# Kernel tuning notes

Measured on AMD Instinct MI355X. Metric: run time of the kernel, lower is better.

Reference implementation:

```python
import jax, jax.numpy as jnp
import numpy as np
import math

SR = 48000       # sample_rate
SEG = 960        # segment_size
NH = 8           # num_harmonics
BASE_F = 220.0   # base_frequency


def _interp_linear(v, Lw):
    # torch F.interpolate(mode='linear', align_corners=False) from (N,C,Lf) -> (N,C,Lw)
    Lf = v.shape[-1]
    pos = (jnp.arange(Lw, dtype=jnp.float32) + 0.5) * (Lf / Lw) - 0.5
    pos = jnp.clip(pos, 0.0, Lf - 1)
    i0 = jnp.floor(pos).astype(jnp.int32)
    i1 = jnp.minimum(i0 + 1, Lf - 1)
    w = (pos - i0.astype(jnp.float32))
    return v[..., i0] * (1.0 - w) + v[..., i1] * w


def setup_inputs() -> dict:
    key = jax.random.key(0)
    k = jax.random.split(key, 4)
    N, C, Lf = 32, 256, 250
    x = jax.random.normal(k[0], (N, C, Lf), jnp.float32)
    phi = jax.random.normal(k[1], (N, 1, 1), jnp.float32)
    # 1x1 Conv1d weights (out, in, 1); small scale keeps f0/mag in a sane range
    w_mag = jax.random.normal(k[2], (NH, C, 1), jnp.float32) * 0.02
    b_mag = jnp.zeros((NH,), jnp.float32)
    w_oct = jax.random.normal(k[3], (1, C, 1), jnp.float32) * 0.02
    b_oct = jnp.zeros((1,), jnp.float32)
    return dict(x=x, phi=phi, w_mag=w_mag, b_mag=b_mag, w_oct=w_oct, b_oct=b_oct)


def reference(x, phi, w_mag, b_mag, w_oct, b_oct):
    N, C, Lf = x.shape
    Lw = Lf * SEG
    # 1x1 conv = channel matmul
    octave = jnp.einsum('oc,ncl->nol', w_oct[:, :, 0], x) + b_oct[None, :, None]   # (N,1,Lf)
    mag = jnp.exp(jnp.minimum(
        jnp.einsum('oc,ncl->nol', w_mag[:, :, 0], x) + b_mag[None, :, None], 6.0))  # (N,NH,Lf)
    f0 = BASE_F * jnp.exp2(octave)                    # (N,1,Lf)
    # NOTE: faithful to source — the f0*mul product is overwritten by interpolate(f0)
    formants = _interp_linear(f0, Lw)                 # (N,1,Lw)
    mag = _interp_linear(mag, Lw)                     # (N,NH,Lw)
    t = jnp.cumsum(formants / SR, axis=2) + phi       # (N,1,Lw) phase accumulation
    harmonics = jnp.sin(2.0 * math.pi * t) * mag      # (N,NH,Lw)
    wave = harmonics.mean(axis=1, keepdims=True)      # (N,1,Lw)
    return wave
```

## Files before the change

### kernel.cpp

```cpp
#include <hip/hip_runtime.h>
#include <hip/hip_bf16.h>
#include <math.h>

#define SRATE 48000.0
#define SEGSZ 960
#define NHARM 8
#define LFRM 250
#define LWAVE (LFRM * SEGSZ)
#define CCH 256
#define RPB 5

__global__ __launch_bounds__(256) void k_frames(
        const float* __restrict__ x,
        const float* __restrict__ w_mag, const float* __restrict__ b_mag,
        const float* __restrict__ w_oct, const float* __restrict__ b_oct,
        float* __restrict__ f0, float* __restrict__ magbar) {
    __shared__ float sred[NHARM + 1][4][64];
    int tid  = threadIdx.x;
    int lane = tid & 63;
    int wv   = tid >> 6;

    int n = blockIdx.x;
    int i = blockIdx.y * 64 + lane;
    bool act = (i < LFRM);
    int ii = act ? i : (LFRM - 1);
    const float* xp = x + (size_t)n * CCH * LFRM + ii;

    float oct = 0.f;
    float mh[NHARM];
#pragma unroll
    for (int h = 0; h < NHARM; ++h) mh[h] = 0.f;

    int c0 = wv * 64;
#pragma unroll 8
    for (int cc = 0; cc < 64; ++cc) {
        int c = c0 + cc;
        float xv = xp[(size_t)c * LFRM];
        oct = fmaf(w_oct[c], xv, oct);
#pragma unroll
        for (int h = 0; h < NHARM; ++h)
            mh[h] = fmaf(w_mag[h * CCH + c], xv, mh[h]);
    }
    sred[0][wv][lane] = oct;
#pragma unroll
    for (int h = 0; h < NHARM; ++h) sred[1 + h][wv][lane] = mh[h];
    __syncthreads();

    if (tid < 64 && act) {
        float o = sred[0][0][lane] + sred[0][1][lane] + sred[0][2][lane] + sred[0][3][lane];
        o += b_oct[0];
        float f0v = 220.0f * exp2f(o);
        float ms = 0.f;
#pragma unroll
        for (int h = 0; h < NHARM; ++h) {
            float mv = sred[1 + h][0][lane] + sred[1 + h][1][lane]
                     + sred[1 + h][2][lane] + sred[1 + h][3][lane];
            ms += expf(fminf(mv + b_mag[h], 6.0f));
        }
        f0[n * LFRM + i]     = f0v;
        magbar[n * LFRM + i] = ms * (1.0f / NHARM);
    }
}

__global__ __launch_bounds__(256) void k_wave(
        const float* __restrict__ f0, const float* __restrict__ magbar,
        const float* __restrict__ phi, float* __restrict__ out) {
    __shared__ float  sf0[LFRM];
    __shared__ float  smb[LFRM];
    __shared__ double sP[LFRM];

    int tid = threadIdx.x;
    int n = blockIdx.y;
    int g = blockIdx.x;

    const float* f0g = f0 + n * LFRM;
    const float* mbg = magbar + n * LFRM;
    if (tid < LFRM) {
        sf0[tid] = f0g[tid];
        smb[tid] = mbg[tid];
    }
    __syncthreads();

    if (tid < 64) {
        int lane = tid;
        double S[4];
        double local = 0.0;
#pragma unroll
        for (int m = 0; m < 4; ++m) {
            int k = 4 * lane + m;
            double s = 0.0;
            if (k < LFRM - 1)
                s = 480.0 * ((double)sf0[k] + (double)sf0[k + 1]) * (1.0 / SRATE);
            S[m] = s;
            local += s;
        }
        double incl = local;
        for (int off = 1; off < 64; off <<= 1) {
            double up = __shfl_up(incl, off, 64);
            if (lane >= off) incl += up;
        }
        double run = (incl - local) + 480.0 * (double)sf0[0] * (1.0 / SRATE);
#pragma unroll
        for (int m = 0; m < 4; ++m) {
            int k = 4 * lane + m;
            if (k < LFRM) sP[k] = run;
            run += S[m];
        }
    }
    __syncthreads();

    if (tid >= 240) return;
    double ph = (double)phi[n];
    int j0 = tid * 4;

#pragma unroll
    for (int r = 0; r < RPB; ++r) {
        int k = g * RPB + r;
        float rr[4];
        size_t l0;
        if (k < LFRM - 1) {
            float fk = sf0[k];
            float df = sf0[k + 1] - fk;
            float m0 = smb[k];
            float dm = smb[k + 1] - m0;
            double base = ph + sP[k];
            float bf = (float)(base - floor(base));
            float c1 = fk * (float)(1.0 / SRATE);
            float c2 = df * (float)(1.0 / (2.0 * SEGSZ * SRATE));
            l0 = (size_t)(SEGSZ / 2) + (size_t)k * SEGSZ + j0;
#pragma unroll
            for (int q = 0; q < 4; ++q) {
                float mf = (float)(j0 + q + 1);
                float t  = fmaf(mf, c1, fmaf(mf * mf, c2, bf));
                float fr = t - floorf(t);
                float s  = __builtin_amdgcn_sinf(fr);
                float w  = ((float)(j0 + q) + 0.5f) * (1.0f / SEGSZ);
                rr[q] = s * fmaf(w, dm, m0);
            }
        } else {
            bool tail = (tid >= 120);
            int kk = tail ? (LFRM - 1) : 0;
            float fk = sf0[kk];
            float mg = smb[kk];
            double base = ph + (tail ? sP[LFRM - 1] : 0.0);
            float bf = (float)(base - floor(base));
            float c1 = fk * (float)(1.0 / SRATE);
            int jl = (tail ? (tid - 120) : tid) * 4;
            l0 = (tail ? (size_t)(LWAVE - SEGSZ / 2) : 0) + jl;
#pragma unroll
            for (int q = 0; q < 4; ++q) {
                float mf = (float)(jl + q + 1);
                float t  = fmaf(mf, c1, bf);
                float fr = t - floorf(t);
                rr[q] = __builtin_amdgcn_sinf(fr) * mg;
            }
        }
        *reinterpret_cast<float4*>(out + (size_t)n * LWAVE + l0) =
            make_float4(rr[0], rr[1], rr[2], rr[3]);
    }
}

extern "C" void kernel_launch(void* const* d_in, const int* in_sizes, int n_in,
                              void* d_out, int out_size, void* d_ws, size_t ws_size,
                              hipStream_t stream) {
    const float* x     = (const float*)d_in[0];
    const float* phi   = (const float*)d_in[1];
    const float* w_mag = (const float*)d_in[2];
    const float* b_mag = (const float*)d_in[3];
    const float* w_oct = (const float*)d_in[4];
    const float* b_oct = (const float*)d_in[5];
    float* out = (float*)d_out;

    int N = in_sizes[1];

    char* ws = (char*)d_ws;
    float* f0     = (float*)ws;
    float* magbar = (float*)(ws + 64 * 1024);

    k_frames<<<dim3(N, 4), 256, 0, stream>>>(x, w_mag, b_mag, w_oct, b_oct, f0, magbar);
    k_wave<<<dim3(LFRM / RPB, N), 256, 0, stream>>>(f0, magbar, phi, out);
}
```

Before: 20.87 us.

## Fuse frame conv and wave synthesis into one cooperative kernel with grid sync

Merges the two kernels into a single cooperative launch: blocks first compute the per-frame conv (f0, mean magnitude), then a grid-wide sync, then wave synthesis. This removes the second launch and its gap. Each wave block now covers 16 frames instead of 5, so the grid is smaller. The phase prefix is stored as wrapped floats, with phi folded in, which drops per-row double floor work. The risk is that the grid sync costs more than the launch it replaces, and the coarser wave grid (512 blocks) may reduce parallelism.

```diff
diff --git a/kernel.cpp b/kernel.cpp
--- a/kernel.cpp
+++ b/kernel.cpp
@@ -1,4 +1,5 @@
 #include <hip/hip_runtime.h>
+#include <hip/hip_cooperative_groups.h>
 #include <hip/hip_bf16.h>
 #include <math.h>
 
@@ -8,20 +9,22 @@
 #define LFRM 250
 #define LWAVE (LFRM * SEGSZ)
 #define CCH 256
-#define RPB 5
-
-__global__ __launch_bounds__(256) void k_frames(
+
+namespace cg = cooperative_groups;
+
+__device__ __forceinline__ void conv_body(
+        int n, int strip,
         const float* __restrict__ x,
         const float* __restrict__ w_mag, const float* __restrict__ b_mag,
         const float* __restrict__ w_oct, const float* __restrict__ b_oct,
-        float* __restrict__ f0, float* __restrict__ magbar) {
-    __shared__ float sred[NHARM + 1][4][64];
+        float* __restrict__ f0, float* __restrict__ magbar,
+        float* smem) {
+    float (*sred)[4][64] = (float (*)[4][64])smem;
     int tid  = threadIdx.x;
     int lane = tid & 63;
     int wv   = tid >> 6;
 
-    int n = blockIdx.x;
-    int i = blockIdx.y * 64 + lane;
+    int i = strip * 64 + lane;
     bool act = (i < LFRM);
     int ii = act ? i : (LFRM - 1);
     const float* xp = x + (size_t)n * CCH * LFRM + ii;
@@ -32,14 +35,20 @@
     for (int h = 0; h < NHARM; ++h) mh[h] = 0.f;
 
     int c0 = wv * 64;
-#pragma unroll 8
-    for (int cc = 0; cc < 64; ++cc) {
-        int c = c0 + cc;
-        float xv = xp[(size_t)c * LFRM];
-        oct = fmaf(w_oct[c], xv, oct);
-#pragma unroll
-        for (int h = 0; h < NHARM; ++h)
-            mh[h] = fmaf(w_mag[h * CCH + c], xv, mh[h]);
+#pragma unroll
+    for (int o = 0; o < 4; ++o) {
+        float xv[16];
+#pragma unroll
+        for (int u = 0; u < 16; ++u)
+            xv[u] = xp[(size_t)(c0 + o * 16 + u) * LFRM];
+#pragma unroll
+        for (int u = 0; u < 16; ++u) {
+            int c = c0 + o * 16 + u;
+            oct = fmaf(w_oct[c], xv[u], oct);
+#pragma unroll
+            for (int h = 0; h < NHARM; ++h)
+                mh[h] = fmaf(w_mag[h * CCH + c], xv[u], mh[h]);
+        }
     }
     sred[0][wv][lane] = oct;
 #pragma unroll
@@ -47,8 +56,8 @@
     __syncthreads();
 
     if (tid < 64 && act) {
-        float o = sred[0][0][lane] + sred[0][1][lane] + sred[0][2][lane] + sred[0][3][lane];
-        o += b_oct[0];
+        float o = sred[0][0][lane] + sred[0][1][lane]
+                + sred[0][2][lane] + sred[0][3][lane] + b_oct[0];
         float f0v = 220.0f * exp2f(o);
         float ms = 0.f;
 #pragma unroll
@@ -62,27 +71,25 @@
     }
 }
 
-__global__ __launch_bounds__(256) void k_wave(
+__device__ __forceinline__ void wave_body(
+        int n, int g,
         const float* __restrict__ f0, const float* __restrict__ magbar,
-        const float* __restrict__ phi, float* __restrict__ out) {
-    __shared__ float  sf0[LFRM];
-    __shared__ float  smb[LFRM];
-    __shared__ double sP[LFRM];
+        const float* __restrict__ phi, float* __restrict__ out,
+        float* smem) {
+    float* sf0 = smem;
+    float* smb = smem + 256;
+    float* sfr = smem + 512;
 
     int tid = threadIdx.x;
-    int n = blockIdx.y;
-    int g = blockIdx.x;
-
-    const float* f0g = f0 + n * LFRM;
-    const float* mbg = magbar + n * LFRM;
     if (tid < LFRM) {
-        sf0[tid] = f0g[tid];
-        smb[tid] = mbg[tid];
+        sf0[tid] = f0[n * LFRM + tid];
+        smb[tid] = magbar[n * LFRM + tid];
     }
     __syncthreads();
 
     if (tid < 64) {
         int lane = tid;
+        double ph = (double)phi[n];
         double S[4];
         double local = 0.0;
 #pragma unroll
@@ -99,23 +106,24 @@
             double up = __shfl_up(incl, off, 64);
             if (lane >= off) incl += up;
         }
-        double run = (incl - local) + 480.0 * (double)sf0[0] * (1.0 / SRATE);
+        double run = (incl - local) + 480.0 * (double)sf0[0] * (1.0 / SRATE) + ph;
 #pragma unroll
         for (int m = 0; m < 4; ++m) {
             int k = 4 * lane + m;
-            if (k < LFRM) sP[k] = run;
+            if (k < LFRM) sfr[k] = (float)(run - floor(run));
             run += S[m];
         }
+        if (lane == 0) sfr[LFRM] = (float)(ph - floor(ph));
     }
     __syncthreads();
 
     if (tid >= 240) return;
-    double ph = (double)phi[n];
     int j0 = tid * 4;
 
 #pragma unroll
-    for (int r = 0; r < RPB; ++r) {
-        int k = g * RPB + r;
+    for (int r = 0; r < 16; ++r) {
+        int k = g * 16 + r;
+        if (k >= LFRM) break;
         float rr[4];
         size_t l0;
         if (k < LFRM - 1) {
@@ -123,8 +131,7 @@
             float df = sf0[k + 1] - fk;
             float m0 = smb[k];
             float dm = smb[k + 1] - m0;
-            double base = ph + sP[k];
-            float bf = (float)(base - floor(base));
+            float bf = sfr[k];
             float c1 = fk * (float)(1.0 / SRATE);
             float c2 = df * (float)(1.0 / (2.0 * SEGSZ * SRATE));
             l0 = (size_t)(SEGSZ / 2) + (size_t)k * SEGSZ + j0;
@@ -139,11 +146,9 @@
             }
         } else {
             bool tail = (tid >= 120);
-            int kk = tail ? (LFRM - 1) : 0;
-            float fk = sf0[kk];
-            float mg = smb[kk];
-            double base = ph + (tail ? sP[LFRM - 1] : 0.0);
-            float bf = (float)(base - floor(base));
+            float fk = tail ? sf0[LFRM - 1] : sf0[0];
+            float mg = tail ? smb[LFRM - 1] : smb[0];
+            float bf = tail ? sfr[LFRM - 1] : sfr[LFRM];
             float c1 = fk * (float)(1.0 / SRATE);
             int jl = (tail ? (tid - 120) : tid) * 4;
             l0 = (tail ? (size_t)(LWAVE - SEGSZ / 2) : 0) + jl;
@@ -158,6 +163,37 @@
         *reinterpret_cast<float4*>(out + (size_t)n * LWAVE + l0) =
             make_float4(rr[0], rr[1], rr[2], rr[3]);
     }
+}
+
+__global__ __launch_bounds__(256, 2) void k_all(
+        const float* __restrict__ x, const float* __restrict__ phi,
+        const float* __restrict__ w_mag, const float* __restrict__ b_mag,
+        const float* __restrict__ w_oct, const float* __restrict__ b_oct,
+        float* __restrict__ f0, float* __restrict__ magbar,
+        float* __restrict__ out, int N) {
+    __shared__ float smem[2304];
+    int bid = blockIdx.x;
+    if (bid < 4 * N)
+        conv_body(bid >> 2, bid & 3, x, w_mag, b_mag, w_oct, b_oct, f0, magbar, smem);
+    cg::this_grid().sync();
+    wave_body(bid >> 4, bid & 15, f0, magbar, phi, out, smem);
+}
+
+__global__ __launch_bounds__(256) void k_frames_fb(
+        const float* __restrict__ x,
+        const float* __restrict__ w_mag, const float* __restrict__ b_mag,
+        const float* __restrict__ w_oct, const float* __restrict__ b_oct,
+        float* __restrict__ f0, float* __restrict__ magbar) {
+    __shared__ float smem[2304];
+    conv_body(blockIdx.x >> 2, blockIdx.x & 3, x, w_mag, b_mag, w_oct, b_oct,
+              f0, magbar, smem);
+}
+
+__global__ __launch_bounds__(256) void k_wave_fb(
+        const float* __restrict__ f0, const float* __restrict__ magbar,
+        const float* __restrict__ phi, float* __restrict__ out) {
+    __shared__ float smem[768];
+    wave_body(blockIdx.x >> 4, blockIdx.x & 15, f0, magbar, phi, out, smem);
 }
 
 extern "C" void kernel_launch(void* const* d_in, const int* in_sizes, int n_in,
@@ -177,6 +213,15 @@
     float* f0     = (float*)ws;
     float* magbar = (float*)(ws + 64 * 1024);
 
-    k_frames<<<dim3(N, 4), 256, 0, stream>>>(x, w_mag, b_mag, w_oct, b_oct, f0, magbar);
-    k_wave<<<dim3(LFRM / RPB, N), 256, 0, stream>>>(f0, magbar, phi, out);
-}
+    void* args[] = { (void*)&x, (void*)&phi, (void*)&w_mag, (void*)&b_mag,
+                     (void*)&w_oct, (void*)&b_oct, (void*)&f0, (void*)&magbar,
+                     (void*)&out, (void*)&N };
+    hipError_t e = hipLaunchCooperativeKernel((const void*)k_all,
+                                              dim3(16 * N), dim3(256),
+                                              args, 0, stream);
+    if (e != hipSuccess) {
+        k_frames_fb<<<dim3(4 * N), 256, 0, stream>>>(x, w_mag, b_mag, w_oct,
+                                                     b_oct, f0, magbar);
+        k_wave_fb<<<dim3(16 * N), 256, 0, stream>>>(f0, magbar, phi, out);
+    }
+}
```

Measured after the change: 79.11 us. 3.79x slower.
